# Kernel optimization log

Hardware: AMD Instinct MI355X
Metric: run time of the kernel (lower is better)

## Reference

```python
import jax, jax.numpy as jnp
import numpy as np

N = 30000
MAXN = 32
IN_DIM = 128
OUT_DIM = 128
NHEAD = 4
HEAD_DIM = OUT_DIM // NHEAD
LN_EPS = 1e-5


def setup_inputs() -> dict:
    key = jax.random.key(0)
    ks = jax.random.split(key, 10)
    h = jax.random.normal(ks[0], (N, IN_DIM), dtype=jnp.float32)
    neighbor_idx = jax.random.randint(ks[1], (N, MAXN), 0, N, dtype=jnp.int64)
    neighbor_mask = jax.random.randint(ks[2], (N, MAXN), 0, 2, dtype=jnp.int32)
    s = 1.0 / np.sqrt(IN_DIM)
    Wq = jax.random.uniform(ks[3], (IN_DIM, OUT_DIM), jnp.float32, -s, s)
    Wk = jax.random.uniform(ks[4], (IN_DIM, OUT_DIM), jnp.float32, -s, s)
    Wv = jax.random.uniform(ks[5], (IN_DIM, OUT_DIM), jnp.float32, -s, s)
    so = 1.0 / np.sqrt(OUT_DIM)
    Wfc = jax.random.uniform(ks[6], (OUT_DIM, OUT_DIM), jnp.float32, -so, so)
    bfc = jax.random.uniform(ks[7], (OUT_DIM,), jnp.float32, -so, so)
    gamma = jnp.ones((OUT_DIM,), jnp.float32)
    beta = jnp.zeros((OUT_DIM,), jnp.float32)
    return {"h": h, "Wq": Wq, "Wk": Wk, "Wv": Wv, "Wfc": Wfc, "bfc": bfc,
            "gamma": gamma, "beta": beta,
            "neighbor_idx": neighbor_idx, "neighbor_mask": neighbor_mask}


def reference(h, Wq, Wk, Wv, Wfc, bfc, gamma, beta, neighbor_idx, neighbor_mask):
    n = h.shape[0]
    Q = h @ Wq                                   # [N, out_dim]
    Kh = (h @ Wk).reshape(n, NHEAD, HEAD_DIM)     # [N, H, D]
    Vh = (h @ Wv).reshape(n, NHEAD, HEAD_DIM)
    Qh = Q.reshape(n, NHEAD, HEAD_DIM)
    K_neigh = Kh[neighbor_idx]                    # [N, M, H, D] irregular gather
    V_neigh = Vh[neighbor_idx]                    # [N, M, H, D]
    scores = jnp.einsum('nhd,nmhd->nmh', Qh, K_neigh) / np.sqrt(HEAD_DIM)
    scores = jnp.where(neighbor_mask[:, :, None] == 0, jnp.float32(-1e9), scores)
    alpha = jax.nn.softmax(scores, axis=1)        # softmax over neighbors
    out_heads = jnp.einsum('nmh,nmhd->nhd', alpha, V_neigh).reshape(n, OUT_DIM)
    # res_proj is None since in_dim == out_dim -> residual is Q; dropout p=0 (eval)
    out = jax.nn.gelu(out_heads @ Wfc + bfc + Q, approximate=False)
    mean = jnp.mean(out, axis=-1, keepdims=True)
    var = jnp.mean(jnp.square(out - mean), axis=-1, keepdims=True)
    out = (out - mean) * jax.lax.rsqrt(var + LN_EPS) * gamma + beta
    return out
```

## Files before the change

### kernel.cpp

```cpp
#include <hip/hip_runtime.h>
#include <hip/hip_fp16.h>
#include <math.h>

#define N_NODES 30000
#define MAXN 32
#define DIM 128
#define NHEAD 4
#define HDIM 32
#define LN_EPS 1e-5f

typedef _Float16 f16;
typedef unsigned char uchar;
typedef __attribute__((ext_vector_type(8))) _Float16 f16x8;
typedef __attribute__((ext_vector_type(4))) float f32x4;
typedef __attribute__((ext_vector_type(2))) float f32x2;

static __device__ __forceinline__ __half2 as_h2(uint u) { return __builtin_bit_cast(__half2, u); }
static __device__ __forceinline__ uint as_u(__half2 h) { return __builtin_bit_cast(uint, h); }
static __device__ __forceinline__ f16x8 as_f16x8(uint4 u) { return __builtin_bit_cast(f16x8, u); }

static __device__ __forceinline__ void async_ld16(const uint* g, uint* lds_base) {
    __builtin_amdgcn_global_load_lds(
        (const __attribute__((address_space(1))) void*)g,
        (__attribute__((address_space(3))) void*)lds_base,
        16, 0, 0);
}

__global__ __launch_bounds__(128) void prep_kernel(
    const float* __restrict__ Wq, const float* __restrict__ Wk,
    const float* __restrict__ Wv, const float* __restrict__ Wfc,
    f16* __restrict__ WqT, f16* __restrict__ WkT,
    f16* __restrict__ WvT, f16* __restrict__ WfcT)
{
    const int n = blockIdx.x, k = threadIdx.x;
    WqT[n * DIM + k]  = (f16)Wq[k * DIM + n];
    WkT[n * DIM + k]  = (f16)Wk[k * DIM + n];
    WvT[n * DIM + k]  = (f16)Wv[k * DIM + n];
    WfcT[n * DIM + k] = (f16)Wfc[k * DIM + n];
}

__global__ __launch_bounds__(256) void qkv_mfma_kernel(
    const float* __restrict__ h,
    const f16* __restrict__ WqT,
    const f16* __restrict__ WkT,
    const f16* __restrict__ WvT,
    f16* __restrict__ Qout,
    uchar* __restrict__ Kout8,
    uchar* __restrict__ Vout8)
{
    __shared__ f16 wlds[DIM][136];

    const int lane = threadIdx.x & 63;
    const int wid  = threadIdx.x >> 6;
    const int r0w  = blockIdx.x * 64 + wid * 16;
    const int rl = lane & 15;
    const int kb = lane >> 4;

    const int arow = min(r0w + rl, N_NODES - 1);
    const float* hrow = h + (size_t)arow * DIM + kb * 8;
    f16x8 a[4];
#pragma unroll
    for (int ks = 0; ks < 4; ++ks) {
        float4 f0 = *(const float4*)(hrow + ks * 32);
        float4 f1 = *(const float4*)(hrow + ks * 32 + 4);
        f16x8 v;
        v[0] = (f16)f0.x; v[1] = (f16)f0.y; v[2] = (f16)f0.z; v[3] = (f16)f0.w;
        v[4] = (f16)f1.x; v[5] = (f16)f1.y; v[6] = (f16)f1.z; v[7] = (f16)f1.w;
        a[ks] = v;
    }

    f32x4 acc[8];

#define STAGE_W(WT)                                                         \
    {                                                                       \
        const uint4* s4 = (const uint4*)(WT);                               \
        _Pragma("unroll")                                                   \
        for (int i = 0; i < 8; ++i) {                                       \
            int L = i * 256 + (int)threadIdx.x;                             \
            *(uint4*)(&wlds[L >> 4][(L & 15) * 8]) = s4[L];                 \
        }                                                                   \
    }

#define GEMM_LDS()                                                          \
    _Pragma("unroll")                                                       \
    for (int tc = 0; tc < 8; ++tc) acc[tc] = (f32x4){0.f, 0.f, 0.f, 0.f};   \
    _Pragma("unroll")                                                       \
    for (int ks = 0; ks < 4; ++ks) {                                        \
        _Pragma("unroll")                                                   \
        for (int tc = 0; tc < 8; ++tc) {                                    \
            f16x8 bfrag = *(const f16x8*)(&wlds[rl + 16 * tc][ks * 32 + kb * 8]); \
            acc[tc] = __builtin_amdgcn_mfma_f32_16x16x32_f16(a[ks], bfrag, acc[tc], 0, 0, 0); \
        }                                                                   \
    }

#define STORE_FP8(OUT)                                                      \
    _Pragma("unroll")                                                       \
    for (int j = 0; j < 4; ++j) {                                           \
        const int row = r0w + kb * 4 + j;                                   \
        if (row < N_NODES) {                                                \
            uchar* orow = (OUT) + (size_t)row * DIM;                        \
            _Pragma("unroll")                                               \
            for (int tc = 0; tc < 8; ++tc) {                                \
                uint r = (uint)__builtin_amdgcn_cvt_pk_fp8_f32(acc[tc][j], 0.f, 0, false); \
                orow[rl + 16 * tc] = (uchar)(r & 0xffu);                    \
            }                                                               \
        }                                                                   \
    }

    STAGE_W(WqT);
    __syncthreads();
    GEMM_LDS();
#pragma unroll
    for (int j = 0; j < 4; ++j) {
        const int row = r0w + kb * 4 + j;
        if (row < N_NODES) {
            f16* orow = Qout + (size_t)row * DIM;
#pragma unroll
            for (int tc = 0; tc < 8; ++tc) orow[rl + 16 * tc] = (f16)acc[tc][j];
        }
    }
    __syncthreads();
    STAGE_W(WkT);
    __syncthreads();
    GEMM_LDS();
    STORE_FP8(Kout8);
    __syncthreads();
    STAGE_W(WvT);
    __syncthreads();
    GEMM_LDS();
    STORE_FP8(Vout8);
}

__global__ __launch_bounds__(512, 6) void attn_fc_kernel(
    const f16* __restrict__ Qh,
    const uchar* __restrict__ K8,
    const uchar* __restrict__ V8,
    const int* __restrict__ nidx,
    const int* __restrict__ nmask,
    const f16* __restrict__ WfcT,
    const float* __restrict__ bfc,
    const float* __restrict__ gamma,
    const float* __restrict__ beta,
    float* __restrict__ out)
{
    __shared__ uint  vlds8[8][1024];
    __shared__ uint  qsh[8][68];
    __shared__ float al_f[8][NHEAD][33];
    __shared__ uint  rv_u[8][68];
    __shared__ float fcout[8][132];
    __shared__ int   idx_s[8][MAXN];

    const int t    = threadIdx.x;
    const int b    = blockIdx.x;
    const int w    = t >> 6;
    const int lane = t & 63;
    const int node = b * 8 + w;

    const int m   = lane & 31;
    const int hh2 = lane >> 5;
    const int src = nidx[(size_t)node * MAXN + m];
    const int msk = nmask[(size_t)node * MAXN + m];
    qsh[w][lane] = ((const uint*)Qh)[(size_t)node * 64 + lane];
    if (lane < 32) idx_s[w][m] = src;

    const uint4* k8r0 = (const uint4*)(K8 + (size_t)src * DIM + hh2 * HDIM);
    const uint4* k8r1 = (const uint4*)(K8 + (size_t)src * DIM + (hh2 + 2) * HDIM);
    uint4 ka0 = k8r0[0], ka1 = k8r0[1];
    uint4 kb0 = k8r1[0], kb1 = k8r1[1];

    {
#pragma unroll
        for (int i = 0; i < 4; ++i) {
            int r = i * 8 + (lane >> 3);
            int c = lane & 7;
            const uint* gp = (const uint*)(V8 + (size_t)idx_s[w][r] * DIM + c * 16);
            async_ld16(gp, &vlds8[w][i * 256]);
        }
    }

    float sc[2];
#pragma unroll
    for (int hp = 0; hp < 2; ++hp) {
        const int hh = hh2 + 2 * hp;
        uint kw[8];
        if (hp == 0) {
            kw[0] = ka0.x; kw[1] = ka0.y; kw[2] = ka0.z; kw[3] = ka0.w;
            kw[4] = ka1.x; kw[5] = ka1.y; kw[6] = ka1.z; kw[7] = ka1.w;
        } else {
            kw[0] = kb0.x; kw[1] = kb0.y; kw[2] = kb0.z; kw[3] = kb0.w;
            kw[4] = kb1.x; kw[5] = kb1.y; kw[6] = kb1.z; kw[7] = kb1.w;
        }
        const uint* qu = &qsh[w][hh * 16];
        float acc = 0.f;
#pragma unroll
        for (int i = 0; i < 8; ++i) {
            f32x2 v01 = __builtin_amdgcn_cvt_pk_f32_fp8(kw[i], false);
            f32x2 v23 = __builtin_amdgcn_cvt_pk_f32_fp8(kw[i], true);
            float2 q01 = __half22float2(as_h2(qu[2 * i]));
            float2 q23 = __half22float2(as_h2(qu[2 * i + 1]));
            acc = fmaf(q01.x, v01.x, acc);
            acc = fmaf(q01.y, v01.y, acc);
            acc = fmaf(q23.x, v23.x, acc);
            acc = fmaf(q23.y, v23.y, acc);
        }
        sc[hp] = (msk == 0) ? -1e9f : acc * 0.17677669529663687f;
    }

#pragma unroll
    for (int hp = 0; hp < 2; ++hp) {
        float mx = sc[hp];
#pragma unroll
        for (int off = 1; off < 32; off <<= 1)
            mx = fmaxf(mx, __shfl_xor(mx, off));
        float e = __expf(sc[hp] - mx);
        float s = e;
#pragma unroll
        for (int off = 1; off < 32; off <<= 1)
            s += __shfl_xor(s, off);
        al_f[w][hh2 + 2 * hp][m] = e / s;
    }

    asm volatile("s_waitcnt vmcnt(0)" ::: "memory");
    {
        const int hh = lane >> 4;
        const uint sh = (lane & 1) ? 16u : 0u;
        float a0 = 0.f, a1 = 0.f;
#pragma unroll
        for (int mm = 0; mm < MAXN; ++mm) {
            uint u = vlds8[w][mm * 32 + (lane >> 1)];
            f32x2 vf = __builtin_amdgcn_cvt_pk_f32_fp8(u >> sh, false);
            float al = al_f[w][hh][mm];
            a0 = fmaf(al, vf.x, a0);
            a1 = fmaf(al, vf.y, a1);
        }
        rv_u[w][lane] = as_u(__floats2half2_rn(a0, a1));
    }
    __syncthreads();

    {
        const int rl  = lane & 15;
        const int kb  = lane >> 4;
        const int col = 16 * w + rl;

        f32x4 acc = (f32x4){0.f, 0.f, 0.f, 0.f};
#pragma unroll
        for (int ks = 0; ks < 4; ++ks) {
            uint4 au = *(const uint4*)(&rv_u[rl & 7][ks * 16 + kb * 4]);
            if (rl >= 8) au = (uint4){0u, 0u, 0u, 0u};
            f16x8 af = as_f16x8(au);
            f16x8 bfr = *(const f16x8*)(WfcT + (size_t)col * DIM + ks * 32 + kb * 8);
            acc = __builtin_amdgcn_mfma_f32_16x16x32_f16(af, bfr, acc, 0, 0, 0);
        }
        if (kb < 2) {
#pragma unroll
            for (int j = 0; j < 4; ++j) fcout[kb * 4 + j][col] = acc[j];
        }
    }
    __syncthreads();

    {
        float g2[2];
        float s1 = 0.f, s2 = 0.f;
#pragma unroll
        for (int p = 0; p < 2; ++p) {
            const int c = lane + 64 * p;
            __half2 qh2 = as_h2(qsh[w][c >> 1]);
            float qv = __half2float((c & 1) ? __high2half(qh2) : __low2half(qh2));
            float x = fcout[w][c] + bfc[c] + qv;
            float gg = 0.5f * x * (1.0f + erff(x * 0.70710678118654752f));
            g2[p] = gg;
            s1 += gg;
            s2 += gg * gg;
        }
#pragma unroll
        for (int off = 1; off < 64; off <<= 1) {
            s1 += __shfl_xor(s1, off);
            s2 += __shfl_xor(s2, off);
        }
        float mean = s1 * (1.0f / DIM);
        float var  = s2 * (1.0f / DIM) - mean * mean;
        float invs = rsqrtf(var + LN_EPS);
#pragma unroll
        for (int p = 0; p < 2; ++p) {
            const int c = lane + 64 * p;
            out[(size_t)node * DIM + c] = (g2[p] - mean) * invs * gamma[c] + beta[c];
        }
    }
}

extern "C" void kernel_launch(void* const* d_in, const int* in_sizes, int n_in,
                              void* d_out, int out_size, void* d_ws, size_t ws_size,
                              hipStream_t stream) {
    (void)in_sizes; (void)n_in; (void)out_size; (void)ws_size;
    const float* h     = (const float*)d_in[0];
    const float* Wq    = (const float*)d_in[1];
    const float* Wk    = (const float*)d_in[2];
    const float* Wv    = (const float*)d_in[3];
    const float* Wfc   = (const float*)d_in[4];
    const float* bfc   = (const float*)d_in[5];
    const float* gamma = (const float*)d_in[6];
    const float* beta  = (const float*)d_in[7];
    const int* nidx    = (const int*)d_in[8];
    const int* nmask   = (const int*)d_in[9];

    f16*   Qh   = (f16*)d_ws;
    uchar* K8   = (uchar*)(Qh + (size_t)N_NODES * DIM);
    uchar* V8   = K8 + (size_t)N_NODES * DIM;
    f16*   WqT  = (f16*)(V8 + (size_t)N_NODES * DIM);
    f16*   WkT  = WqT + (size_t)DIM * DIM;
    f16*   WvT  = WkT + (size_t)DIM * DIM;
    f16*   WfcT = WvT + (size_t)DIM * DIM;

    prep_kernel<<<DIM, DIM, 0, stream>>>(Wq, Wk, Wv, Wfc, WqT, WkT, WvT, WfcT);
    qkv_mfma_kernel<<<(N_NODES + 63) / 64, 256, 0, stream>>>(h, WqT, WkT, WvT, Qh, K8, V8);
    attn_fc_kernel<<<N_NODES / 8, 512, 0, stream>>>(Qh, K8, V8, nidx, nmask,
                                                    WfcT, bfc, gamma, beta, (float*)d_out);
}
```

Measured before the change: 70.29 us.

## Compact masked neighbors to skip gathering and accumulating masked V rows

Uses a wave ballot and ds_permute to move valid neighbor indices to the front, then gathers V rows only for the valid count and runs the alpha·V loop only over that count. Masked entries get -inf, which lets the softmax max reduction be dropped, and an all-masked row falls back to uniform weights. Q is now stored as fp32 instead of fp16, which doubles Q traffic but removes the conversions. The cost is a data-dependent loop trip count and extra shuffle work in place of a fixed unrolled loop.

```diff
diff --git a/kernel.cpp b/kernel.cpp
--- a/kernel.cpp
+++ b/kernel.cpp
@@ -44,7 +44,7 @@
     const f16* __restrict__ WqT,
     const f16* __restrict__ WkT,
     const f16* __restrict__ WvT,
-    f16* __restrict__ Qout,
+    float* __restrict__ Qout,
     uchar* __restrict__ Kout8,
     uchar* __restrict__ Vout8)
 {
@@ -114,9 +114,9 @@
     for (int j = 0; j < 4; ++j) {
         const int row = r0w + kb * 4 + j;
         if (row < N_NODES) {
-            f16* orow = Qout + (size_t)row * DIM;
-#pragma unroll
-            for (int tc = 0; tc < 8; ++tc) orow[rl + 16 * tc] = (f16)acc[tc][j];
+            float* orow = Qout + (size_t)row * DIM;
+#pragma unroll
+            for (int tc = 0; tc < 8; ++tc) orow[rl + 16 * tc] = acc[tc][j];
         }
     }
     __syncthreads();
@@ -132,7 +132,7 @@
 }
 
 __global__ __launch_bounds__(512, 6) void attn_fc_kernel(
-    const f16* __restrict__ Qh,
+    const float* __restrict__ Qf,
     const uchar* __restrict__ K8,
     const uchar* __restrict__ V8,
     const int* __restrict__ nidx,
@@ -144,11 +144,10 @@
     float* __restrict__ out)
 {
     __shared__ uint  vlds8[8][1024];
-    __shared__ uint  qsh[8][68];
+    __shared__ float qsh[8][132];
     __shared__ float al_f[8][NHEAD][33];
     __shared__ uint  rv_u[8][68];
     __shared__ float fcout[8][132];
-    __shared__ int   idx_s[8][MAXN];
 
     const int t    = threadIdx.x;
     const int b    = blockIdx.x;
@@ -160,20 +159,32 @@
     const int hh2 = lane >> 5;
     const int src = nidx[(size_t)node * MAXN + m];
     const int msk = nmask[(size_t)node * MAXN + m];
-    qsh[w][lane] = ((const uint*)Qh)[(size_t)node * 64 + lane];
-    if (lane < 32) idx_s[w][m] = src;
-
-    const uint4* k8r0 = (const uint4*)(K8 + (size_t)src * DIM + hh2 * HDIM);
-    const uint4* k8r1 = (const uint4*)(K8 + (size_t)src * DIM + (hh2 + 2) * HDIM);
+    {
+        float2 q2 = ((const float2*)(Qf + (size_t)node * DIM))[lane];
+        *(float2*)(&qsh[w][2 * lane]) = q2;
+    }
+
+    const uint vm  = (uint)__ballot(msk != 0);
+    const int  nv0 = __popc(vm);
+    const bool am  = (nv0 == 0);
+    const int  nv  = am ? MAXN : nv0;
+    const uint below = (1u << m) - 1u;
+    const int  pos = msk ? __popc(vm & below) : (nv0 + __popc((~vm) & below));
+    const int srcC = __builtin_amdgcn_ds_permute(((lane & 32) + pos) << 2, src);
+    const int kSrc = (m < nv) ? srcC : 0;
+
+    const uint4* k8r0 = (const uint4*)(K8 + (size_t)kSrc * DIM + hh2 * HDIM);
+    const uint4* k8r1 = (const uint4*)(K8 + (size_t)kSrc * DIM + (hh2 + 2) * HDIM);
     uint4 ka0 = k8r0[0], ka1 = k8r0[1];
     uint4 kb0 = k8r1[0], kb1 = k8r1[1];
 
     {
-#pragma unroll
-        for (int i = 0; i < 4; ++i) {
+        const int nchunk = (nv + 7) >> 3;
+        for (int i = 0; i < nchunk; ++i) {
             int r = i * 8 + (lane >> 3);
-            int c = lane & 7;
-            const uint* gp = (const uint*)(V8 + (size_t)idx_s[w][r] * DIM + c * 16);
+            int srcR = __shfl(srcC, (lane & 32) | r);
+            srcR = (r < nv) ? srcR : 0;
+            const uint* gp = (const uint*)(V8 + (size_t)srcR * DIM + (lane & 7) * 16);
             async_ld16(gp, &vlds8[w][i * 256]);
         }
     }
@@ -190,29 +201,26 @@
             kw[0] = kb0.x; kw[1] = kb0.y; kw[2] = kb0.z; kw[3] = kb0.w;
             kw[4] = kb1.x; kw[5] = kb1.y; kw[6] = kb1.z; kw[7] = kb1.w;
         }
-        const uint* qu = &qsh[w][hh * 16];
+        const float2* qf2 = (const float2*)(&qsh[w][hh * HDIM]);
         float acc = 0.f;
 #pragma unroll
         for (int i = 0; i < 8; ++i) {
             f32x2 v01 = __builtin_amdgcn_cvt_pk_f32_fp8(kw[i], false);
             f32x2 v23 = __builtin_amdgcn_cvt_pk_f32_fp8(kw[i], true);
-            float2 q01 = __half22float2(as_h2(qu[2 * i]));
-            float2 q23 = __half22float2(as_h2(qu[2 * i + 1]));
+            float2 q01 = qf2[2 * i];
+            float2 q23 = qf2[2 * i + 1];
             acc = fmaf(q01.x, v01.x, acc);
             acc = fmaf(q01.y, v01.y, acc);
             acc = fmaf(q23.x, v23.x, acc);
             acc = fmaf(q23.y, v23.y, acc);
         }
-        sc[hp] = (msk == 0) ? -1e9f : acc * 0.17677669529663687f;
+        float sv = acc * 0.17677669529663687f;
+        sc[hp] = am ? 0.f : ((m < nv0) ? sv : -INFINITY);
     }
 
 #pragma unroll
     for (int hp = 0; hp < 2; ++hp) {
-        float mx = sc[hp];
-#pragma unroll
-        for (int off = 1; off < 32; off <<= 1)
-            mx = fmaxf(mx, __shfl_xor(mx, off));
-        float e = __expf(sc[hp] - mx);
+        float e = __expf(sc[hp]);
         float s = e;
 #pragma unroll
         for (int off = 1; off < 32; off <<= 1)
@@ -225,8 +233,7 @@
         const int hh = lane >> 4;
         const uint sh = (lane & 1) ? 16u : 0u;
         float a0 = 0.f, a1 = 0.f;
-#pragma unroll
-        for (int mm = 0; mm < MAXN; ++mm) {
+        for (int mm = 0; mm < nv; ++mm) {
             uint u = vlds8[w][mm * 32 + (lane >> 1)];
             f32x2 vf = __builtin_amdgcn_cvt_pk_f32_fp8(u >> sh, false);
             float al = al_f[w][hh][mm];
@@ -264,9 +271,7 @@
 #pragma unroll
         for (int p = 0; p < 2; ++p) {
             const int c = lane + 64 * p;
-            __half2 qh2 = as_h2(qsh[w][c >> 1]);
-            float qv = __half2float((c & 1) ? __high2half(qh2) : __low2half(qh2));
-            float x = fcout[w][c] + bfc[c] + qv;
+            float x = fcout[w][c] + bfc[c] + qsh[w][c];
             float gg = 0.5f * x * (1.0f + erff(x * 0.70710678118654752f));
             g2[p] = gg;
             s1 += gg;
@@ -303,8 +308,8 @@
     const int* nidx    = (const int*)d_in[8];
     const int* nmask   = (const int*)d_in[9];
 
-    f16*   Qh   = (f16*)d_ws;
-    uchar* K8   = (uchar*)(Qh + (size_t)N_NODES * DIM);
+    float* Qf   = (float*)d_ws;
+    uchar* K8   = (uchar*)(Qf + (size_t)N_NODES * DIM);
     uchar* V8   = K8 + (size_t)N_NODES * DIM;
     f16*   WqT  = (f16*)(V8 + (size_t)N_NODES * DIM);
     f16*   WkT  = WqT + (size_t)DIM * DIM;
@@ -312,7 +317,7 @@
     f16*   WfcT = WvT + (size_t)DIM * DIM;
 
     prep_kernel<<<DIM, DIM, 0, stream>>>(Wq, Wk, Wv, Wfc, WqT, WkT, WvT, WfcT);
-    qkv_mfma_kernel<<<(N_NODES + 63) / 64, 256, 0, stream>>>(h, WqT, WkT, WvT, Qh, K8, V8);
-    attn_fc_kernel<<<N_NODES / 8, 512, 0, stream>>>(Qh, K8, V8, nidx, nmask,
+    qkv_mfma_kernel<<<(N_NODES + 63) / 64, 256, 0, stream>>>(h, WqT, WkT, WvT, Qf, K8, V8);
+    attn_fc_kernel<<<N_NODES / 8, 512, 0, stream>>>(Qf, K8, V8, nidx, nmask,
                                                     WfcT, bfc, gamma, beta, (float*)d_out);
 }
```

Result: faster. 64.19 us (-8.7%).
